# Kernel tuning notes

Measured on AMD Instinct MI355X. Metric: run time of the kernel, lower is better.

The kernel has to match this reference:

```python
import jax, jax.numpy as jnp
import numpy as np

P_DIMS = [512, 256, 128]
K_DIMS = [256, 256, 256]
NT = 65536


def setup_inputs() -> dict:
    key = jax.random.key(0)
    ks = jax.random.split(key, 8 * len(P_DIMS))
    inp = {}
    ki = 0
    for i, (p, k) in enumerate(zip(P_DIMS, K_DIMS)):
        inp[f"x{i}"] = jax.random.normal(ks[ki], (NT, p), jnp.float32); ki += 1
        inp[f"alpha{i}"] = jax.random.normal(ks[ki], (1, k), jnp.float32); ki += 1
        inp[f"beta{i}"] = jax.random.normal(ks[ki], (k, p), jnp.float32) * 0.05; ki += 1
        inp[f"sig{i}"] = jax.random.normal(ks[ki], (1, k), jnp.float32); ki += 1
        inp[f"eta{i}"] = jax.random.normal(ks[ki], (1, k), jnp.float32); ki += 1
        inp[f"gam{i}"] = jax.random.normal(ks[ki], (k, 1), jnp.float32) * 0.03; ki += 1
        inp[f"w{i}"] = jax.random.normal(ks[ki], (k, p), jnp.float32); ki += 1
        inp[f"disc{i}"] = jnp.array([3.0], jnp.float32); ki += 1
    return inp


def _source(x, alpha, beta, sig, eta, gam, w, disc):
    # x: (nt,p); w,beta: (k,p); alpha,sig,eta: (1,k); gam: (k,1); disc: (1,)
    h = eta ** 2                                           # (1,k)
    d2 = (jnp.sum(x * x, axis=1, keepdims=True)
          - 2.0 * (x @ w.T)
          + jnp.sum(w * w, axis=1)[None, :])
    a = jnp.exp(-(gam[:, 0] ** 2)[None, :] * d2)           # (nt,k)
    ah = a * h                                             # a * H
    hx = jnp.sum(ah, axis=1)                               # (nt,)
    mu = x @ beta.T + alpha                                # (nt,k)
    mux = jnp.sum(mu * ah, axis=1) / hx
    sig2x = jnp.sum((sig ** 2) * (ah ** 2), axis=1) / (hx * hx)
    hx_dc = hx * jax.nn.sigmoid(disc[0])
    return mux, sig2x, hx, hx_dc


def reference(x0, alpha0, beta0, sig0, eta0, gam0, w0, disc0,
              x1, alpha1, beta1, sig1, eta1, gam1, w1, disc1,
              x2, alpha2, beta2, sig2, eta2, gam2, w2, disc2):
    srcs = [
        (x0, alpha0, beta0, sig0, eta0, gam0, w0, disc0),
        (x1, alpha1, beta1, sig1, eta1, gam1, w1, disc1),
        (x2, alpha2, beta2, sig2, eta2, gam2, w2, disc2),
    ]
    outs = [_source(*s) for s in srcs]  # fixed small loop over sources
    mux_t = jnp.stack([o[0] for o in outs])     # (S,nt)
    sig2x_t = jnp.stack([o[1] for o in outs])
    hx_t = jnp.stack([o[2] for o in outs])
    hx_dc = jnp.stack([o[3] for o in outs])
    denom = jnp.sum(hx_dc, axis=0)
    mux_comb = jnp.sum(mux_t * hx_dc, axis=0) / denom
    sig2x_comb = jnp.sum(sig2x_t * hx_dc ** 2, axis=0) / (denom ** 2)
    mux_final = jnp.concatenate([mux_t, mux_comb[None]], axis=0)      # (S+1,nt)
    sig2x_final = jnp.concatenate([sig2x_t, sig2x_comb[None]], axis=0)
    hx_final = jnp.concatenate([hx_t, denom[None]], axis=0)
    return (mux_final, sig2x_final, hx_final)
```

## Files before the change

kernel.cpp:

```cpp
#include <hip/hip_runtime.h>
#include <hip/hip_bf16.h>

typedef __attribute__((ext_vector_type(8))) short short8;
typedef __attribute__((ext_vector_type(4))) float f32x4;

#define NT 65536

__device__ __forceinline__ unsigned short f2bf(float f) {
    union { float f; unsigned int u; } v; v.f = f;
    unsigned int u = v.u;
    unsigned int r = (u + 0x7fffu + ((u >> 16) & 1u)) >> 16;
    return (unsigned short)r;
}

__device__ __forceinline__ unsigned int cvt_pk_bf16(float lo, float hi) {
    unsigned int r;
    asm("v_cvt_pk_bf16_f32 %0, %1, %2" : "=v"(r) : "v"(lo), "v"(hi));
    return r;
}

#define LGKM0()  asm volatile("s_waitcnt lgkmcnt(0)" ::: "memory")
#define VMCNT6() asm volatile("s_waitcnt vmcnt(6)" ::: "memory")
#define VMCNT0() asm volatile("s_waitcnt vmcnt(0)" ::: "memory")
#define BAR()    __builtin_amdgcn_s_barrier()
#define SB0()    __builtin_amdgcn_sched_barrier(0)

__global__ void prep_kernel(const float* __restrict__ w0, const float* __restrict__ b0,
                            const float* __restrict__ a0, const float* __restrict__ s0,
                            const float* __restrict__ e0, const float* __restrict__ g0,
                            const float* __restrict__ w1, const float* __restrict__ b1,
                            const float* __restrict__ a1, const float* __restrict__ s1,
                            const float* __restrict__ e1, const float* __restrict__ g1,
                            const float* __restrict__ w2, const float* __restrict__ b2,
                            const float* __restrict__ a2, const float* __restrict__ s2,
                            const float* __restrict__ e2, const float* __restrict__ g2,
                            unsigned short* __restrict__ bc, float* __restrict__ prmAll) {
    __shared__ float red[2];
    const int bx = blockIdx.x;
    const int s = bx >> 9;
    const int n = bx & 511;
    const int P = 512 >> s;
    const float* w   = (s == 0) ? w0 : ((s == 1) ? w1 : w2);
    const float* bet = (s == 0) ? b0 : ((s == 1) ? b1 : b2);
    const float* alp = (s == 0) ? a0 : ((s == 1) ? a1 : a2);
    const float* sig = (s == 0) ? s0 : ((s == 1) ? s1 : s2);
    const float* eta = (s == 0) ? e0 : ((s == 1) ? e1 : e2);
    const float* gam = (s == 0) ? g0 : ((s == 1) ? g1 : g2);
    unsigned short* dstb = bc + ((s == 0) ? 0 : ((s == 1) ? (512 * 512) : (512 * 512 + 512 * 256)));
    float* prm = prmAll + 1280 * s;

    const int tid = threadIdx.x;
    const int k16 = n >> 5;
    const int typ = (n >> 4) & 1;
    const int k = k16 * 16 + (n & 15);
    const bool isw = (typ == 0);
    const float* src = (isw ? w : bet) + (size_t)k * P;
    unsigned short* dst = dstb + (size_t)n * P;
    float ss = 0.f;
    for (int c = tid; c < P; c += 128) {
        float f = src[c];
        dst[c] = f2bf(f);
        if (isw) ss += f * f;
    }
#pragma unroll
    for (int m = 1; m < 64; m <<= 1) ss += __shfl_xor(ss, m);
    if ((tid & 63) == 0) red[tid >> 6] = ss;
    __syncthreads();
    if (isw && tid == 0) prm[k] = red[0] + red[1];
    if (n == 0) {
        for (int kk = tid; kk < 256; kk += 128) {
            float g = gam[kk], e = eta[kk];
            prm[256 + kk]  = g * g;
            prm[512 + kk]  = e * e;
            prm[768 + kk]  = alp[kk];
            prm[1024 + kk] = sig[kk] * sig[kk];
        }
    }
}

template<int P>
__global__ __launch_bounds__(256, 3)
void fused_src(const float* __restrict__ x, const unsigned short* __restrict__ Bc,
               const float* __restrict__ prm, float* __restrict__ pwsS) {
    constexpr int NK = P / 32;
    __shared__ unsigned short Bs[2][128 * 32];
    __shared__ unsigned short Xs[128 * 32];
    __shared__ float xn2[128];

    const int b = blockIdx.x;
    const int xt = (b >> 5) * 8 + (b & 7);
    const int pt = (b >> 3) & 3;

    const int tid = threadIdx.x, lane = tid & 63, wv = tid >> 6;
    const int wp = wv >> 1, wx = wv & 1;
    const int l15 = lane & 15, l4 = lane >> 4;

    const int srow = tid >> 1, shalf = tid & 1;
    const float* xbase = x + (size_t)(xt * 128 + srow) * P + shalf * 16;

    f32x4 acc[4][4];
#pragma unroll
    for (int pf = 0; pf < 4; pf++)
#pragma unroll
        for (int xf = 0; xf < 4; xf++) acc[pf][xf] = (f32x4){0.f, 0.f, 0.f, 0.f};

    float4 xra[4], xrb[4];
    float ss = 0.f;

    auto gloadB = [&](int nb, int t) {
#pragma unroll
        for (int i = 0; i < 2; i++) {
            const int u = i * 256 + tid;
            const int row = u >> 2;
            const int sl = (u & 3) ^ ((row >> 1) & 3);
            const unsigned short* src = Bc + (size_t)(pt * 128 + row) * P + t * 32 + sl * 8;
            __builtin_amdgcn_global_load_lds((const __attribute__((address_space(1))) void*)src,
                (__attribute__((address_space(3))) void*)&Bs[nb][(i * 256 + wv * 64) * 8], 16, 0, 0);
        }
    };
    auto loadX = [&](float4* xr, int t) {
#pragma unroll
        for (int i = 0; i < 4; i++) xr[i] = *(const float4*)(xbase + t * 32 + i * 4);
    };
    auto cvtWrite = [&](const float4* xr) {
        const int sw = (srow >> 1) & 3;
#pragma unroll
        for (int hh = 0; hh < 2; hh++) {
            float4 q0 = xr[2 * hh], q1 = xr[2 * hh + 1];
            ss += q0.x*q0.x + q0.y*q0.y + q0.z*q0.z + q0.w*q0.w
                + q1.x*q1.x + q1.y*q1.y + q1.z*q1.z + q1.w*q1.w;
            uint4 pk = { cvt_pk_bf16(q0.x, q0.y), cvt_pk_bf16(q0.z, q0.w),
                         cvt_pk_bf16(q1.x, q1.y), cvt_pk_bf16(q1.z, q1.w) };
            const int phys = (shalf * 2 + hh) ^ sw;
            *(uint4*)(&Xs[srow * 32 + phys * 8]) = pk;
        }
    };
    auto compute = [&](int buf) {
        short8 af[4], bf[4];
#pragma unroll
        for (int pf = 0; pf < 4; pf++) {
            const int row = 64 * wp + 16 * pf + l15;
            af[pf] = *(const short8*)(&Bs[buf][row * 32 + ((l4 ^ ((row >> 1) & 3)) << 3)]);
        }
#pragma unroll
        for (int xf = 0; xf < 4; xf++) {
            const int row = 64 * wx + 16 * xf + l15;
            bf[xf] = *(const short8*)(&Xs[row * 32 + ((l4 ^ ((row >> 1) & 3)) << 3)]);
        }
#pragma unroll
        for (int pf = 0; pf < 4; pf++)
#pragma unroll
            for (int xf = 0; xf < 4; xf++)
                acc[pf][xf] = __builtin_amdgcn_mfma_f32_16x16x32_bf16(af[pf], bf[xf], acc[pf][xf], 0, 0, 0);
    };

    gloadB(0, 0);
    loadX(xra, 0);

#pragma unroll 1
    for (int t = 0; t < NK; t += 2) {
        gloadB((t + 1) & 1, t + 1);
        loadX(xrb, t + 1);
        cvtWrite(xra);
        VMCNT6(); LGKM0(); SB0(); BAR(); SB0();
        compute(t & 1);
        SB0(); BAR(); SB0();
        const bool more = (t + 2 < NK);
        if (more) {
            gloadB(t & 1, t + 2);
            loadX(xra, t + 2);
        }
        cvtWrite(xrb);
        if (more) { VMCNT6(); } else { VMCNT0(); }
        LGKM0(); SB0(); BAR(); SB0();
        compute((t + 1) & 1);
        SB0(); BAR(); SB0();
    }

    ss += __shfl_xor(ss, 1);
    if (shalf == 0) xn2[srow] = ss;
    __syncthreads();

    const int kb0 = (pt * 4 + 2 * wp) * 16 + 4 * l4;
    f32x4 wn2[2], g2[2], hv[2], alv[2], s2v[2];
#pragma unroll
    for (int K = 0; K < 2; K++) {
        const int kk = kb0 + 16 * K;
        wn2[K] = *(const f32x4*)(prm + kk);
        g2[K]  = *(const f32x4*)(prm + 256 + kk);
        hv[K]  = *(const f32x4*)(prm + 512 + kk);
        alv[K] = *(const f32x4*)(prm + 768 + kk);
        s2v[K] = *(const f32x4*)(prm + 1024 + kk);
    }
    float (*part)[128][3] = (float (*)[128][3])(&Xs[0]);
#pragma unroll
    for (int xf = 0; xf < 4; xf++) {
        const int xrow = 64 * wx + 16 * xf + l15;
        const float xv = xn2[xrow];
        float hs = 0.f, ms = 0.f, gs = 0.f;
#pragma unroll
        for (int K = 0; K < 2; K++) {
#pragma unroll
            for (int j = 0; j < 4; j++) {
                const float aw = acc[2 * K][xf][j];
                const float ab = acc[2 * K + 1][xf][j];
                const float d2 = xv - 2.f * aw + wn2[K][j];
                const float a  = __expf(-g2[K][j] * d2);
                const float ah = a * hv[K][j];
                hs += ah;
                ms += (ab + alv[K][j]) * ah;
                gs += s2v[K][j] * ah * ah;
            }
        }
        hs += __shfl_xor(hs, 16); hs += __shfl_xor(hs, 32);
        ms += __shfl_xor(ms, 16); ms += __shfl_xor(ms, 32);
        gs += __shfl_xor(gs, 16); gs += __shfl_xor(gs, 32);
        if (l4 == 0) {
            part[wp][xrow][0] = hs;
            part[wp][xrow][1] = ms;
            part[wp][xrow][2] = gs;
        }
    }
    __syncthreads();
    if (tid < 128) {
        const int gr = xt * 128 + tid;
#pragma unroll
        for (int v = 0; v < 3; v++)
            pwsS[(size_t)(pt * 3 + v) * NT + gr] = part[0][tid][v] + part[1][tid][v];
    }
}

__global__ void combine_kernel(const float* __restrict__ pws,
                               const float* __restrict__ d0, const float* __restrict__ d1,
                               const float* __restrict__ d2, float* __restrict__ out) {
    const int t = blockIdx.x * 256 + threadIdx.x;
    float mux[3], s2x[3], hx[3];
#pragma unroll
    for (int s = 0; s < 3; s++) {
        const float* bbase = pws + (size_t)s * 12 * NT;
        float hh = 0.f, mm = 0.f, gg = 0.f;
#pragma unroll
        for (int pt = 0; pt < 4; pt++) {
            hh += bbase[(size_t)(pt * 3 + 0) * NT + t];
            mm += bbase[(size_t)(pt * 3 + 1) * NT + t];
            gg += bbase[(size_t)(pt * 3 + 2) * NT + t];
        }
        mux[s] = mm / hh; s2x[s] = gg / (hh * hh); hx[s] = hh;
        out[(size_t)s * NT + t]       = mux[s];
        out[(size_t)(4 + s) * NT + t] = s2x[s];
        out[(size_t)(8 + s) * NT + t] = hh;
    }
    const float sd0 = 1.f / (1.f + __expf(-d0[0]));
    const float sd1 = 1.f / (1.f + __expf(-d1[0]));
    const float sd2 = 1.f / (1.f + __expf(-d2[0]));
    const float c0 = hx[0] * sd0, c1 = hx[1] * sd1, c2 = hx[2] * sd2;
    const float den = c0 + c1 + c2;
    const float muc = mux[0] * c0 + mux[1] * c1 + mux[2] * c2;
    const float sgc = s2x[0] * c0 * c0 + s2x[1] * c1 * c1 + s2x[2] * c2 * c2;
    out[(size_t)3 * NT + t]  = muc / den;
    out[(size_t)7 * NT + t]  = sgc / (den * den);
    out[(size_t)11 * NT + t] = den;
}

extern "C" void kernel_launch(void* const* d_in, const int* in_sizes, int n_in,
                              void* d_out, int out_size, void* d_ws, size_t ws_size,
                              hipStream_t stream) {
    const float* x0 = (const float*)d_in[0];
    const float* x1 = (const float*)d_in[8];
    const float* x2 = (const float*)d_in[16];

    unsigned short* bc = (unsigned short*)d_ws;
    float* prmAll = (float*)((char*)d_ws + 917504);
    float* pws    = (float*)((char*)d_ws + 917504 + 15360);
    float* out = (float*)d_out;

    prep_kernel<<<1536, 128, 0, stream>>>(
        (const float*)d_in[6],  (const float*)d_in[2],  (const float*)d_in[1],
        (const float*)d_in[3],  (const float*)d_in[4],  (const float*)d_in[5],
        (const float*)d_in[14], (const float*)d_in[10], (const float*)d_in[9],
        (const float*)d_in[11], (const float*)d_in[12], (const float*)d_in[13],
        (const float*)d_in[22], (const float*)d_in[18], (const float*)d_in[17],
        (const float*)d_in[19], (const float*)d_in[20], (const float*)d_in[21],
        bc, prmAll);

    const size_t bcoff1 = 512 * 512, bcoff2 = 512 * 512 + 512 * 256;
    fused_src<512><<<2048, 256, 0, stream>>>(x0, bc,          prmAll,        pws);
    fused_src<256><<<2048, 256, 0, stream>>>(x1, bc + bcoff1, prmAll + 1280, pws + (size_t)12 * NT);
    fused_src<128><<<2048, 256, 0, stream>>>(x2, bc + bcoff2, prmAll + 2560, pws + (size_t)24 * NT);
    combine_kernel<<<256, 256, 0, stream>>>(pws, (const float*)d_in[7], (const float*)d_in[15],
                                            (const float*)d_in[23], out);
}
```

Measured before the change: 130.4 us.

## Deepen the GEMM load pipeline to three tiles in flight with quad-buffered LDS

Replaces the two-stage ping-pong main loop with a fully unrolled software pipeline. Up to three K-tiles of B (async global-to-LDS) and X (register prefetch) are in flight, using four B buffers in LDS and double-buffered X in LDS. The explicit vmcnt waits are dropped; ordering now relies on compiler-inserted waits on the X register loads, which are issued after the matching B loads. The goal is to hide more global-memory latency per barrier step. In exchange, LDS use roughly doubles and the extra prefetch registers raise register pressure at the 3-blocks-per-CU launch bound.

```diff
diff --git a/kernel.cpp b/kernel.cpp
--- a/kernel.cpp
+++ b/kernel.cpp
@@ -20,8 +20,6 @@
 }
 
 #define LGKM0()  asm volatile("s_waitcnt lgkmcnt(0)" ::: "memory")
-#define VMCNT6() asm volatile("s_waitcnt vmcnt(6)" ::: "memory")
-#define VMCNT0() asm volatile("s_waitcnt vmcnt(0)" ::: "memory")
 #define BAR()    __builtin_amdgcn_s_barrier()
 #define SB0()    __builtin_amdgcn_sched_barrier(0)
 
@@ -83,8 +81,8 @@
 void fused_src(const float* __restrict__ x, const unsigned short* __restrict__ Bc,
                const float* __restrict__ prm, float* __restrict__ pwsS) {
     constexpr int NK = P / 32;
-    __shared__ unsigned short Bs[2][128 * 32];
-    __shared__ unsigned short Xs[128 * 32];
+    __shared__ unsigned short Bs[4][128 * 32];
+    __shared__ unsigned short Xs[2][128 * 32];
     __shared__ float xn2[128];
 
     const int b = blockIdx.x;
@@ -104,7 +102,7 @@
 #pragma unroll
         for (int xf = 0; xf < 4; xf++) acc[pf][xf] = (f32x4){0.f, 0.f, 0.f, 0.f};
 
-    float4 xra[4], xrb[4];
+    float4 xr[4][4];
     float ss = 0.f;
 
     auto gloadB = [&](int nb, int t) {
@@ -118,34 +116,34 @@
                 (__attribute__((address_space(3))) void*)&Bs[nb][(i * 256 + wv * 64) * 8], 16, 0, 0);
         }
     };
-    auto loadX = [&](float4* xr, int t) {
-#pragma unroll
-        for (int i = 0; i < 4; i++) xr[i] = *(const float4*)(xbase + t * 32 + i * 4);
-    };
-    auto cvtWrite = [&](const float4* xr) {
+    auto loadX = [&](float4* xrs, int t) {
+#pragma unroll
+        for (int i = 0; i < 4; i++) xrs[i] = *(const float4*)(xbase + t * 32 + i * 4);
+    };
+    auto cvtWrite = [&](const float4* xrs, int xb) {
         const int sw = (srow >> 1) & 3;
 #pragma unroll
         for (int hh = 0; hh < 2; hh++) {
-            float4 q0 = xr[2 * hh], q1 = xr[2 * hh + 1];
+            float4 q0 = xrs[2 * hh], q1 = xrs[2 * hh + 1];
             ss += q0.x*q0.x + q0.y*q0.y + q0.z*q0.z + q0.w*q0.w
                 + q1.x*q1.x + q1.y*q1.y + q1.z*q1.z + q1.w*q1.w;
             uint4 pk = { cvt_pk_bf16(q0.x, q0.y), cvt_pk_bf16(q0.z, q0.w),
                          cvt_pk_bf16(q1.x, q1.y), cvt_pk_bf16(q1.z, q1.w) };
             const int phys = (shalf * 2 + hh) ^ sw;
-            *(uint4*)(&Xs[srow * 32 + phys * 8]) = pk;
-        }
-    };
-    auto compute = [&](int buf) {
+            *(uint4*)(&Xs[xb][srow * 32 + phys * 8]) = pk;
+        }
+    };
+    auto compute = [&](int bb, int xb) {
         short8 af[4], bf[4];
 #pragma unroll
         for (int pf = 0; pf < 4; pf++) {
             const int row = 64 * wp + 16 * pf + l15;
-            af[pf] = *(const short8*)(&Bs[buf][row * 32 + ((l4 ^ ((row >> 1) & 3)) << 3)]);
+            af[pf] = *(const short8*)(&Bs[bb][row * 32 + ((l4 ^ ((row >> 1) & 3)) << 3)]);
         }
 #pragma unroll
         for (int xf = 0; xf < 4; xf++) {
             const int row = 64 * wx + 16 * xf + l15;
-            bf[xf] = *(const short8*)(&Xs[row * 32 + ((l4 ^ ((row >> 1) & 3)) << 3)]);
+            bf[xf] = *(const short8*)(&Xs[xb][row * 32 + ((l4 ^ ((row >> 1) & 3)) << 3)]);
         }
 #pragma unroll
         for (int pf = 0; pf < 4; pf++)
@@ -154,26 +152,27 @@
                 acc[pf][xf] = __builtin_amdgcn_mfma_f32_16x16x32_bf16(af[pf], bf[xf], acc[pf][xf], 0, 0, 0);
     };
 
-    gloadB(0, 0);
-    loadX(xra, 0);
-
-#pragma unroll 1
-    for (int t = 0; t < NK; t += 2) {
-        gloadB((t + 1) & 1, t + 1);
-        loadX(xrb, t + 1);
-        cvtWrite(xra);
-        VMCNT6(); LGKM0(); SB0(); BAR(); SB0();
-        compute(t & 1);
-        SB0(); BAR(); SB0();
-        const bool more = (t + 2 < NK);
-        if (more) {
-            gloadB(t & 1, t + 2);
-            loadX(xra, t + 2);
-        }
-        cvtWrite(xrb);
-        if (more) { VMCNT6(); } else { VMCNT0(); }
+#pragma unroll
+    for (int d = 0; d < 3; d++) {
+        if (d < NK) {
+            gloadB(d, d); SB0();
+            loadX(xr[d], d); SB0();
+        }
+    }
+    cvtWrite(xr[0], 0);
+    LGKM0(); SB0(); BAR(); SB0();
+
+#pragma unroll
+    for (int t = 0; t < NK; t++) {
+        if (t + 3 < NK) {
+            gloadB((t + 3) & 3, t + 3); SB0();
+            loadX(xr[(t + 3) & 3], t + 3); SB0();
+        }
+        if (t + 1 < NK) {
+            cvtWrite(xr[(t + 1) & 3], (t + 1) & 1);
+        }
         LGKM0(); SB0(); BAR(); SB0();
-        compute((t + 1) & 1);
+        compute(t & 3, t & 1);
         SB0(); BAR(); SB0();
     }
 
@@ -192,7 +191,7 @@
         alv[K] = *(const f32x4*)(prm + 768 + kk);
         s2v[K] = *(const f32x4*)(prm + 1024 + kk);
     }
-    float (*part)[128][3] = (float (*)[128][3])(&Xs[0]);
+    float (*part)[128][3] = (float (*)[128][3])(&Bs[0][0]);
 #pragma unroll
     for (int xf = 0; xf < 4; xf++) {
         const int xrow = 64 * wx + 16 * xf + l15;
```

New measurement: 126.1 us. -3.3%, faster.
